# Performance work log

Measured on AMD Instinct MI355X. Metric: run time of the kernel, lower is better.

Reference implementation:

```python
import jax, jax.numpy as jnp
import numpy as np

B, C3, Dz, H, W = 2, 128, 32, 24, 24
C2, K = 96, 8
E, NH = 256, 4
HD = E // NH
BETA_ADJ = 0.5
EPS = 1e-5
TOPO_HIDDEN = 64


def setup_inputs() -> dict:
    key = jax.random.key(0)
    ks = jax.random.split(key, 10)
    def n(k, shape, s=0.02):
        return jax.random.normal(k, shape, jnp.float32) * s
    return {
        "F3": jax.random.normal(ks[0], (B, C3, Dz, H, W), jnp.float32),
        "F2": jax.random.normal(ks[1], (B, C2, H, W, K), jnp.float32),
        "Wq": n(ks[2], (C3, E)),
        "Wk": n(ks[3], (C2, E)),
        "Wv": n(ks[4], (C2, E)),
        "Wp": n(ks[5], (E, C3)),
        "ln_q_g": jnp.ones((E,), jnp.float32),
        "ln_q_b": jnp.zeros((E,), jnp.float32),
        "ln_kv_g": jnp.ones((E,), jnp.float32),
        "ln_kv_b": jnp.zeros((E,), jnp.float32),
        "conv1_w": n(ks[6], (TOPO_HIDDEN, C2, 3, 3)),
        "bn_g": jnp.ones((TOPO_HIDDEN,), jnp.float32),
        "bn_b": jnp.zeros((TOPO_HIDDEN,), jnp.float32),
        "conv2_w": n(ks[7], (1, TOPO_HIDDEN, 1, 1)),
        "conv2_b": jnp.zeros((1,), jnp.float32),
        "lam": jnp.asarray(0.3, jnp.float32),
        "D0": 128,
        "slab": 16,
    }


def _layernorm(x, g, b):
    m = jnp.mean(x, -1, keepdims=True)
    v = jnp.mean(jnp.square(x - m), -1, keepdims=True)
    return (x - m) * jax.lax.rsqrt(v + EPS) * g + b


def _conv2d(x, w, pad):
    return jax.lax.conv_general_dilated(
        x, w, (1, 1), [(pad, pad), (pad, pad)],
        dimension_numbers=("NCHW", "OIHW", "NCHW"))


def _forward(F3, F2, Wq, Wk, Wv, Wp, ln_q_g, ln_q_b, ln_kv_g, ln_kv_b,
             conv1_w, bn_g, bn_b, conv2_w, conv2_b, lam, D0, slab):
    HW = H * W
    # static slab-index map (D0, slab are Python ints)
    z0 = np.round(np.linspace(0.0, D0 - 1, Dz)).astype(np.int64)
    k_index = np.clip(z0 // slab, 0, K - 1)

    # ---- TopoPriorHead2D (BatchNorm in eval mode, default running stats 0/1) ----
    f2_bkchw = jnp.transpose(F2, (0, 4, 1, 2, 3)).reshape(B * K, C2, H, W)
    h = _conv2d(f2_bkchw, conv1_w, 1)
    h = h * (bn_g / np.float32(np.sqrt(1.0 + EPS)))[None, :, None, None] + bn_b[None, :, None, None]
    h = jax.nn.relu(h)
    p_pred = _conv2d(h, conv2_w, 0) + conv2_b[None, :, None, None]  # [B*K,1,H,W]
    nei = jnp.ones((1, 1, 3, 3), jnp.float32).at[0, 0, 1, 1].set(0.0)
    ps_pred = _conv2d(p_pred, nei, 1)
    topo_map = (p_pred + 0.5 * ps_pred).reshape(B, K, HW)

    # ---- Q/K/V projections + LayerNorm ----
    x2 = jnp.transpose(F2, (0, 4, 2, 3, 1)).reshape(B, K, HW, C2)
    Kall = _layernorm(x2 @ Wk, ln_kv_g, ln_kv_b).reshape(B, K, HW, NH, HD)
    Vall = _layernorm(x2 @ Wv, ln_kv_g, ln_kv_b).reshape(B, K, HW, NH, HD)
    x3 = jnp.transpose(F3, (0, 2, 3, 4, 1)).reshape(B, Dz, HW, C3)
    Qall = _layernorm(x3 @ Wq, ln_q_g, ln_q_b).reshape(B, Dz, HW, NH, HD)

    Oh = jnp.zeros_like(Qall)
    scale = np.float32(1.0 / np.sqrt(HD))
    hw = np.arange(HW)
    for kk in range(K):
        z_ids = np.nonzero(k_index == kk)[0]
        if z_ids.size == 0:
            continue
        cand = [c for c in (kk - 1, kk, kk + 1) if 0 <= c < K]
        L = len(cand)
        slab_bias = jnp.asarray(np.concatenate(
            [np.full(HW, 0.0 if c == kk else -BETA_ADJ, np.float32) for c in cand]))
        Qg = Qall[:, z_ids]                                    # [B,Ds,HW,NH,HD]
        Kc = Kall[:, np.asarray(cand)].reshape(B, L * HW, NH, HD)
        Vc = Vall[:, np.asarray(cand)].reshape(B, L * HW, NH, HD)
        # [B,NH,Ds,HW,M]
        logits = jnp.einsum('bdphc,bmhc->bhdpm', Qg, Kc) * scale
        logits = logits + slab_bias
        # diagonal topo boost: query pixel p attends to same pixel p in slab cand[j]
        diag = jnp.zeros((B, HW, L * HW), logits.dtype)
        for j, c in enumerate(cand):
            diag = diag.at[:, hw, j * HW + hw].add(lam * topo_map[:, c])
        logits = logits + diag[:, None, None]
        attn = jax.nn.softmax(logits, axis=-1)
        Og = jnp.einsum('bhdpm,bmhc->bdphc', attn, Vc)         # [B,Ds,HW,NH,HD]
        Oh = Oh.at[:, z_ids].set(Og)

    Oall = Oh.reshape(B, Dz, HW, E) @ Wp                        # [B,D,HW,C3]
    Oall = jnp.transpose(Oall.reshape(B, Dz, H, W, C3), (0, 4, 1, 2, 3))
    return F3 + Oall


def reference(F3, F2, Wq, Wk, Wv, Wp, ln_q_g, ln_q_b, ln_kv_g, ln_kv_b,
              conv1_w, bn_g, bn_b, conv2_w, conv2_b, lam, D0, slab):
    return _forward(F3, F2, Wq, Wk, Wv, Wp, ln_q_g, ln_q_b, ln_kv_g, ln_kv_b,
                    conv1_w, bn_g, bn_b, conv2_w, conv2_b, lam, D0, slab)
```

## Files before the change

### kernel.cpp

```cpp
#include <hip/hip_runtime.h>

typedef float f32x4 __attribute__((ext_vector_type(4)));
typedef __bf16 bf16x8 __attribute__((ext_vector_type(8)));
typedef unsigned short ushort_t;

#define DEV_INLINE __device__ __forceinline__

constexpr int B_N  = 2;
constexpr int C3_N = 128;
constexpr int C2_N = 96;
constexpr int DZ_N = 32;
constexpr int H_N  = 24;
constexpr int W_N  = 24;
constexpr int K_N  = 8;
constexpr int E_N  = 256;
constexpr int HW_N = 576;

DEV_INLINE unsigned short f2bf(float x) {
  union { __bf16 b; unsigned short u; } v;
  v.b = (__bf16)x;
  return v.u;
}

__global__ __launch_bounds__(384) void topo_conv1(
    const float* __restrict__ F2, const float* __restrict__ W1,
    float* __restrict__ Hp) {
  const int bid = blockIdx.x;
  const int cc = bid & 3;
  const int tg = (bid >> 2) & 3;
  const int bk = bid >> 4;
  const int b = bk >> 3, k = bk & 7;
  const int tid = threadIdx.x;
  const int y = tid >> 4;
  const int tq = tid & 15;

  __shared__ float simg[8][26][28];
  __shared__ float sw[16 * 97];

  float acc[24];
#pragma unroll
  for (int i = 0; i < 24; i++) acc[i] = 0.f;

  float* simgf = &simg[0][0][0];
  for (int i = tid; i < 8 * 26 * 28; i += 384) simgf[i] = 0.f;
  __syncthreads();

  for (int ch = 0; ch < 3; ch++) {
    if (ch) __syncthreads();
    const int c0 = cc * 24 + ch * 8;
    for (int i = tid; i < 8 * 24 * 24; i += 384) {
      int c = i / 576, p = i - c * 576;
      int yy = p / 24, xx = p - yy * 24;
      simg[c][yy + 1][xx + 1] =
          F2[(((b * C2_N + c0 + c) * H_N + yy) * W_N + xx) * K_N + k];
    }
    for (int i = tid; i < 16 * 72; i += 384) {
      int t2 = i / 72, rest = i - t2 * 72;
      int c = rest / 9, q = rest - c * 9;
      sw[t2 * 97 + c * 12 + q] =
          W1[(tg * 16 + t2) * (C2_N * 9) + (c0 + c) * 9 + q];
    }
    __syncthreads();
#pragma unroll 1
    for (int c = 0; c < 8; c++) {
      float w[9];
#pragma unroll
      for (int q = 0; q < 9; q++) w[q] = sw[tq * 97 + c * 12 + q];
#pragma unroll
      for (int dy = 0; dy < 3; dy++) {
        float r[28];
#pragma unroll
        for (int g = 0; g < 7; g++)
          *(float4*)&r[g * 4] = *(const float4*)&simg[c][y + dy][g * 4];
#pragma unroll
        for (int dx = 0; dx < 3; dx++) {
          float wv = w[dy * 3 + dx];
#pragma unroll
          for (int xx = 0; xx < 24; xx++)
            acc[xx] = fmaf(wv, r[xx + dx], acc[xx]);
        }
      }
    }
  }
  const int t = tg * 16 + tq;
  float* dst = &Hp[((cc * 16 + bk) * 64 + t) * HW_N + y * 24];
#pragma unroll
  for (int xx = 0; xx < 24; xx++) dst[xx] = acc[xx];
}

__global__ __launch_bounds__(576) void topo_mid(
    const float* __restrict__ Hp, const float* __restrict__ bn_g,
    const float* __restrict__ bn_b, const float* __restrict__ W2,
    float* __restrict__ part) {
  const int bid = blockIdx.x;
  const int tg = bid & 3, bk = bid >> 2;
  const int p = threadIdx.x;
  const float inv = rsqrtf(1.0f + 1e-5f);
  float acc = 0.f;
#pragma unroll 1
  for (int tt = 0; tt < 16; tt++) {
    const int t = tg * 16 + tt;
    float v = 0.f;
#pragma unroll
    for (int c4 = 0; c4 < 4; c4++)
      v += Hp[((c4 * 16 + bk) * 64 + t) * HW_N + p];
    acc = fmaf(W2[t], fmaxf(fmaf(bn_g[t] * inv, v, bn_b[t]), 0.f), acc);
  }
  part[(bk * 4 + tg) * HW_N + p] = acc;
}

__global__ __launch_bounds__(576) void topo_final2(
    const float* __restrict__ part, const float* __restrict__ b2,
    float* __restrict__ topo) {
  const int bk = blockIdx.x;
  const int p = threadIdx.x;
  __shared__ float pp[26][28];
  float* ppf = &pp[0][0];
  for (int i = p; i < 26 * 28; i += 576) ppf[i] = 0.f;
  float acc = b2[0];
#pragma unroll
  for (int tg = 0; tg < 4; tg++) acc += part[(bk * 4 + tg) * HW_N + p];
  __syncthreads();
  pp[p / 24 + 1][p % 24 + 1] = acc;
  __syncthreads();
  const int yy = p / 24 + 1, xx = p % 24 + 1;
  float s = pp[yy-1][xx-1] + pp[yy-1][xx] + pp[yy-1][xx+1]
          + pp[yy][xx-1]                  + pp[yy][xx+1]
          + pp[yy+1][xx-1] + pp[yy+1][xx] + pp[yy+1][xx+1];
  topo[bk * HW_N + p] = acc + 0.5f * s;
}

__global__ __launch_bounds__(256) void pack_all(
    const float* __restrict__ Wq, const float* __restrict__ Wk,
    const float* __restrict__ Wv, const float* __restrict__ Wp,
    ushort_t* __restrict__ Wqp, ushort_t* __restrict__ Wkp,
    ushort_t* __restrict__ Wvp, ushort_t* __restrict__ Wpp) {
  const int bblk = blockIdx.x, t = threadIdx.x;
  if (bblk < 256) {
    if (t < 128) Wqp[bblk * 128 + t] = f2bf(Wq[t * 256 + bblk]);
  } else if (bblk < 512) {
    const int n = bblk - 256;
    if (t < 96) Wkp[n * 96 + t] = f2bf(Wk[t * 256 + n]);
  } else if (bblk < 768) {
    const int n = bblk - 512;
    if (t < 96) Wvp[n * 96 + t] = f2bf(Wv[t * 256 + n]);
  } else {
    const int c = bblk - 768;
    Wpp[c * 256 + t] = f2bf(Wp[t * 128 + c]);
  }
}

template <int CIN, int MODE>
__global__ __launch_bounds__(256) void proj_mfma(
    const float* __restrict__ src, const ushort_t* __restrict__ Wpk,
    void* __restrict__ outp, const float* __restrict__ g,
    const float* __restrict__ bb,
    int outer, int bStride, int oStride, int pStride, int cStride) {
  __shared__ ushort_t sA[64 * 128];
  __shared__ int sRB[64];
  const int tid = threadIdx.x;
  const int rowG = blockIdx.x * 64;
  if (tid < 64) {
    int rr = rowG + tid;
    int b2 = rr / (outer * HW_N);
    int rem = rr - b2 * outer * HW_N;
    int o = rem / HW_N;
    int p = rem - o * HW_N;
    sRB[tid] = b2 * bStride + o * oStride + p * pStride;
  }
  __syncthreads();
  {
    const int r = tid & 63, kg = tid >> 6;
    constexpr int KC = CIN / 4;
    const float* s0 = src + sRB[r];
#pragma unroll
    for (int i = 0; i < KC; i += 2) {
      const int k = kg * KC + i;
      const float x0 = s0[k * cStride];
      const float x1 = s0[(k + 1) * cStride];
      const unsigned pr = (unsigned)f2bf(x0) | ((unsigned)f2bf(x1) << 16);
      ((unsigned*)sA)[r * 64 + (((k >> 3) + r) & 15) * 4 + ((k & 7) >> 1)] = pr;
    }
  }
  __syncthreads();
  const int wv = tid >> 6, lane = tid & 63;
  const int quad = lane >> 4, col = lane & 15;
  const int m = wv * 16 + col;
  constexpr int KS = CIN / 32;
  bf16x8 xb[KS];
#pragma unroll
  for (int ks = 0; ks < KS; ks++)
    xb[ks] = *(const bf16x8*)&sA[m * 128 + (((ks * 4 + quad) + m) & 15) * 8];
  f32x4 acc[16];
#pragma unroll
  for (int nt = 0; nt < 16; nt++) {
    const ushort_t* wrow = Wpk + (nt * 16 + col) * CIN + quad * 8;
    f32x4 a = (f32x4){0.f, 0.f, 0.f, 0.f};
#pragma unroll
    for (int ks = 0; ks < KS; ks++) {
      bf16x8 wf = *(const bf16x8*)&wrow[ks * 32];
      a = __builtin_amdgcn_mfma_f32_16x16x32_bf16(wf, xb[ks], a, 0, 0, 0);
    }
    acc[nt] = a;
  }
  const int mrow = rowG + m;
  if (MODE == 0) {
    float* dst = (float*)outp + (size_t)mrow * E_N;
#pragma unroll
    for (int nt = 0; nt < 16; nt++)
      *(f32x4*)&dst[nt * 16 + quad * 4] = acc[nt];
  } else {
    float s = 0.f;
#pragma unroll
    for (int nt = 0; nt < 16; nt++)
      s += acc[nt][0] + acc[nt][1] + acc[nt][2] + acc[nt][3];
    s += __shfl_xor(s, 16); s += __shfl_xor(s, 32);
    const float mean = s * (1.f / 256.f);
    float v = 0.f;
#pragma unroll
    for (int nt = 0; nt < 16; nt++)
#pragma unroll
      for (int r = 0; r < 4; r++) {
        const float d = acc[nt][r] - mean;
        v += d * d;
      }
    v += __shfl_xor(v, 16); v += __shfl_xor(v, 32);
    const float rstd = rsqrtf(v * (1.f / 256.f) + 1e-5f);
    if (MODE == 1) {
      const float QS = 0.18033688f;
      ushort_t* dst = (ushort_t*)outp + (size_t)mrow * E_N;
#pragma unroll
      for (int nt = 0; nt < 16; nt++) {
        const int n0 = nt * 16 + quad * 4;
        const float4 gv = *(const float4*)&g[n0];
        const float4 bv = *(const float4*)&bb[n0];
        ushort4 o;
        o.x = f2bf(QS * fmaf((acc[nt][0] - mean) * rstd, gv.x, bv.x));
        o.y = f2bf(QS * fmaf((acc[nt][1] - mean) * rstd, gv.y, bv.y));
        o.z = f2bf(QS * fmaf((acc[nt][2] - mean) * rstd, gv.z, bv.z));
        o.w = f2bf(QS * fmaf((acc[nt][3] - mean) * rstd, gv.w, bv.w));
        *(ushort4*)&dst[n0] = o;
      }
    }
  }
}

__global__ __launch_bounds__(256) void proj_kv(
    const float* __restrict__ F2, const ushort_t* __restrict__ Wkp,
    const ushort_t* __restrict__ Wvp, ushort_t* __restrict__ Kpk,
    ushort_t* __restrict__ Vtp, const float* __restrict__ g,
    const float* __restrict__ bb) {
  __shared__ ushort_t sA[64 * 128];
  __shared__ ushort_t sT[64][264];
  const int tid = threadIdx.x;
  const int rowG = blockIdx.x * 64;
  {
    const int r = tid & 63, kg = tid >> 6;
    const int rr = rowG + r;
    const int b2 = rr / (K_N * HW_N);
    const int rem = rr - b2 * (K_N * HW_N);
    const int k = rem / HW_N;
    const int p = rem - k * HW_N;
    const float* s0 = F2 + (size_t)b2 * (C2_N * HW_N * K_N) + k + p * K_N;
#pragma unroll
    for (int i = 0; i < 24; i += 2) {
      const int kk = kg * 24 + i;
      const float x0 = s0[kk * (HW_N * K_N)];
      const float x1 = s0[(kk + 1) * (HW_N * K_N)];
      const unsigned pr = (unsigned)f2bf(x0) | ((unsigned)f2bf(x1) << 16);
      ((unsigned*)sA)[r * 64 + (((kk >> 3) + r) & 15) * 4 + ((kk & 7) >> 1)] = pr;
    }
  }
  __syncthreads();
  const int wv = tid >> 6, lane = tid & 63;
  const int quad = lane >> 4, col = lane & 15;
  const int m = wv * 16 + col;
  bf16x8 xb[3];
#pragma unroll
  for (int ks = 0; ks < 3; ks++)
    xb[ks] = *(const bf16x8*)&sA[m * 128 + (((ks * 4 + quad) + m) & 15) * 8];

  const int mrow = rowG + m;
  const int bk = mrow / HW_N;
  const int p = mrow - bk * HW_N;
  const int pc = p >> 6, mm = p & 63;

  {
    f32x4 acc[16];
#pragma unroll
    for (int nt = 0; nt < 16; nt++) {
      const ushort_t* wrow = Wkp + (nt * 16 + col) * 96 + quad * 8;
      f32x4 a = (f32x4){0.f, 0.f, 0.f, 0.f};
#pragma unroll
      for (int ks = 0; ks < 3; ks++) {
        bf16x8 wf = *(const bf16x8*)&wrow[ks * 32];
        a = __builtin_amdgcn_mfma_f32_16x16x32_bf16(wf, xb[ks], a, 0, 0, 0);
      }
      acc[nt] = a;
    }
    float s = 0.f;
#pragma unroll
    for (int nt = 0; nt < 16; nt++)
      s += acc[nt][0] + acc[nt][1] + acc[nt][2] + acc[nt][3];
    s += __shfl_xor(s, 16); s += __shfl_xor(s, 32);
    const float mean = s * (1.f / 256.f);
    float v = 0.f;
#pragma unroll
    for (int nt = 0; nt < 16; nt++)
#pragma unroll
      for (int r = 0; r < 4; r++) {
        const float d = acc[nt][r] - mean;
        v += d * d;
      }
    v += __shfl_xor(v, 16); v += __shfl_xor(v, 32);
    const float rstd = rsqrtf(v * (1.f / 256.f) + 1e-5f);
#pragma unroll
    for (int nt = 0; nt < 16; nt++) {
      const int n0 = nt * 16 + quad * 4;
      const float4 gv = *(const float4*)&g[n0];
      const float4 bv = *(const float4*)&bb[n0];
      ushort4 o;
      o.x = f2bf(fmaf((acc[nt][0] - mean) * rstd, gv.x, bv.x));
      o.y = f2bf(fmaf((acc[nt][1] - mean) * rstd, gv.y, bv.y));
      o.z = f2bf(fmaf((acc[nt][2] - mean) * rstd, gv.z, bv.z));
      o.w = f2bf(fmaf((acc[nt][3] - mean) * rstd, gv.w, bv.w));
      const int h = nt >> 2;
      const int grp = ((nt & 3) * 2 + (quad >> 1)) ^ (mm & 7);
      ushort_t* dst = Kpk +
          ((size_t)((bk * 4 + h) * 9 + pc)) * 4096 +
          mm * 64 + grp * 8 + (quad & 1) * 4;
      *(ushort4*)dst = o;
    }
  }

  {
    f32x4 acc[16];
#pragma unroll
    for (int nt = 0; nt < 16; nt++) {
      const ushort_t* wrow = Wvp + (nt * 16 + col) * 96 + quad * 8;
      f32x4 a = (f32x4){0.f, 0.f, 0.f, 0.f};
#pragma unroll
      for (int ks = 0; ks < 3; ks++) {
        bf16x8 wf = *(const bf16x8*)&wrow[ks * 32];
        a = __builtin_amdgcn_mfma_f32_16x16x32_bf16(wf, xb[ks], a, 0, 0, 0);
      }
      acc[nt] = a;
    }
    float s = 0.f;
#pragma unroll
    for (int nt = 0; nt < 16; nt++)
      s += acc[nt][0] + acc[nt][1] + acc[nt][2] + acc[nt][3];
    s += __shfl_xor(s, 16); s += __shfl_xor(s, 32);
    const float mean = s * (1.f / 256.f);
    float v = 0.f;
#pragma unroll
    for (int nt = 0; nt < 16; nt++)
#pragma unroll
      for (int r = 0; r < 4; r++) {
        const float d = acc[nt][r] - mean;
        v += d * d;
      }
    v += __shfl_xor(v, 16); v += __shfl_xor(v, 32);
    const float rstd = rsqrtf(v * (1.f / 256.f) + 1e-5f);
#pragma unroll
    for (int nt = 0; nt < 16; nt++) {
      const int n0 = nt * 16 + quad * 4;
      const float4 gv = *(const float4*)&g[n0];
      const float4 bv = *(const float4*)&bb[n0];
      ushort4 o;
      o.x = f2bf(fmaf((acc[nt][0] - mean) * rstd, gv.x, bv.x));
      o.y = f2bf(fmaf((acc[nt][1] - mean) * rstd, gv.y, bv.y));
      o.z = f2bf(fmaf((acc[nt][2] - mean) * rstd, gv.z, bv.z));
      o.w = f2bf(fmaf((acc[nt][3] - mean) * rstd, gv.w, bv.w));
      *(ushort4*)&sT[m][n0] = o;
    }
  }
  __syncthreads();
  const int hh = tid >> 6, d = tid & 63;
  __attribute__((aligned(16))) ushort_t tmp[64];
#pragma unroll
  for (int k = 0; k < 64; k++) {
    const int pk = (k & 32) + ((k & 4) << 2) + ((k & 24) >> 1) + (k & 3);
    tmp[k] = sT[pk][hh * 64 + d];
  }
  const int chunk = (bk * 4 + hh) * 9 + pc;
  uint4* dst = (uint4*)&Vtp[chunk * 4096 + d * 64];
  const int sw = d & 7;
#pragma unroll
  for (int gg = 0; gg < 8; gg++) dst[gg ^ sw] = ((const uint4*)tmp)[gg];
}

__global__ __launch_bounds__(256) void attn_kernel(
    const ushort_t* __restrict__ Qbf, const ushort_t* __restrict__ Kpk,
    const ushort_t* __restrict__ Vtp, const float* __restrict__ topo,
    const float* __restrict__ lamp, const int* __restrict__ D0p,
    const int* __restrict__ slabp, ushort_t* __restrict__ Obf) {
  const int bid = blockIdx.x;
  const int hb = bid & 7;
  const int h = hb & 3, b = hb >> 2;
  const int zp = (bid >> 3) & 15;
  const int pb = bid >> 7;
  const int p0 = pb * 64;
  const int tid = threadIdx.x;
  const int w = tid >> 6, lane = tid & 63;
  const int quad = lane >> 4, col = lane & 15;
  const int z = zp * 2 + (w >> 1);
  const int th = w & 1;

  const float LOG2E = 1.44269504f;
  const float lam2 = lamp[0] * LOG2E;
  const int D0 = D0p[0], slab = slabp[0];
  const float step = (float)(D0 - 1) / (float)(DZ_N - 1);

  int kkw, kka, kkb;
  {
    int z0 = (int)floorf(fmaf((float)z, step, 0.5f));
    int kv = z0 / slab;
    kkw = kv < 0 ? 0 : (kv > K_N - 1 ? K_N - 1 : kv);
    int z0a = (int)floorf(fmaf((float)(zp * 2), step, 0.5f));
    int z0b = (int)floorf(fmaf((float)(zp * 2 + 1), step, 0.5f));
    int ka = z0a / slab; ka = ka < 0 ? 0 : (ka > K_N - 1 ? K_N - 1 : ka);
    int kb = z0b / slab; kb = kb < 0 ? 0 : (kb > K_N - 1 ? K_N - 1 : kb);
    kka = ka < kb ? ka : kb;
    kkb = ka < kb ? kb : ka;
  }
  const int c_lo = (kka - 1) < 0 ? 0 : (kka - 1);
  const int c_hi = (kkb + 1) > (K_N - 1) ? (K_N - 1) : (kkb + 1);

  __shared__ ushort_t sKV[2][8192];

  auto issue_fill = [&](int buf, int c, int pc) {
    const size_t cb = ((size_t)(((b * K_N + c) * 4 + h) * 9) + pc) * 4096;
#pragma unroll
    for (int j = 0; j < 4; j++) {
      const int seg = (w << 2) + j;
      const ushort_t* gsrc = (w < 2)
          ? (Kpk + cb + seg * 512 + lane * 8)
          : (Vtp + cb + (seg - 8) * 512 + lane * 8);
      ushort_t* ldst = &sKV[buf][seg * 512];
      __builtin_amdgcn_global_load_lds(
          (const __attribute__((address_space(1))) void*)gsrc,
          (__attribute__((address_space(3))) void*)ldst, 16, 0, 0);
    }
  };

  union { ushort_t u[8]; bf16x8 v; } uo;
#pragma unroll
  for (int i = 0; i < 8; i++) uo.u[i] = 0x3F80;
  const bf16x8 vone = uo.v;

  bf16x8 bq[2][2];
  const int qrow0 = (b * DZ_N + z) * HW_N + p0 + th * 32;
#pragma unroll
  for (int t = 0; t < 2; t++) {
    const ushort_t* qp = &Qbf[(qrow0 + t * 16 + col) * E_N + h * 64 + quad * 8];
    bq[t][0] = *(const bf16x8*)qp;
    bq[t][1] = *(const bf16x8*)(qp + 32);
  }

  f32x4 oacc[2][4];
#pragma unroll
  for (int t = 0; t < 2; t++)
#pragma unroll
    for (int dt = 0; dt < 4; dt++) oacc[t][dt] = (f32x4){0.f, 0.f, 0.f, 0.f};
  f32x4 lacc[2];
  lacc[0] = (f32x4){0.f, 0.f, 0.f, 0.f};
  lacc[1] = (f32x4){0.f, 0.f, 0.f, 0.f};

  const int s7 = col & 7;
  const int o1 = (quad ^ s7) * 8;
  const int o2 = ((quad + 4) ^ s7) * 8;

  int buf = 0;
  issue_fill(0, c_lo, 0);

  for (int c = c_lo; c <= c_hi; c++) {
    const bool act = (c >= kkw - 1) && (c <= kkw + 1);
    const float biasE2 = ((c == kkw) ? -20.0f : -20.5f) * LOG2E;
    const f32x4 bias4 = (f32x4){biasE2, biasE2, biasE2, biasE2};
    const float* topoc = &topo[(b * K_N + c) * HW_N + p0];
#pragma unroll 1
    for (int pc = 0; pc < 9; pc++) {
      __syncthreads();
      {
        int pc2 = pc + 1, c2 = c;
        if (pc2 == 9) { pc2 = 0; c2 = c + 1; }
        if (c2 <= c_hi) issue_fill(buf ^ 1, c2, pc2);
      }
      const ushort_t* sKb = &sKV[buf][0];
      const ushort_t* sVb = &sKV[buf][4096];
      buf ^= 1;
      if (!act) continue;

      bf16x8 ka[4][2];
#pragma unroll
      for (int kt = 0; kt < 4; kt++) {
        const ushort_t* kr = sKb + (kt * 16 + col) * 64;
        ka[kt][0] = *(const bf16x8*)(kr + o1);
        ka[kt][1] = *(const bf16x8*)(kr + o2);
      }

      bf16x8 pfrag[2][2];
#pragma unroll
      for (int t = 0; t < 2; t++) {
        f32x4 sv[4];
#pragma unroll
        for (int kt = 0; kt < 4; kt++) {
          f32x4 acc = __builtin_amdgcn_mfma_f32_16x16x32_bf16(
              ka[kt][0], bq[t][0], bias4, 0, 0, 0);
          acc = __builtin_amdgcn_mfma_f32_16x16x32_bf16(
              ka[kt][1], bq[t][1], acc, 0, 0, 0);
          sv[kt] = acc;
        }
        float xv[4][4];
#pragma unroll
        for (int kt = 0; kt < 4; kt++)
#pragma unroll
          for (int r = 0; r < 4; r++)
            xv[kt][r] = sv[kt][r];
        if (pc == pb) {
          const int ctt = th * 2 + t;
          const float tv2 = lam2 * topoc[th * 32 + t * 16 + col];
          const bool qok = ((col >> 2) == quad);
#pragma unroll
          for (int kt = 0; kt < 4; kt++)
#pragma unroll
            for (int r = 0; r < 4; r++)
              xv[kt][r] += (qok && kt == ctt && (col & 3) == r) ? tv2 : 0.f;
        }
        float ev[4][4];
#pragma unroll
        for (int kt = 0; kt < 4; kt++)
#pragma unroll
          for (int r = 0; r < 4; r++)
            ev[kt][r] = __builtin_amdgcn_exp2f(xv[kt][r]);
#pragma unroll
        for (int f = 0; f < 2; f++) {
          union { uint4 u; bf16x8 v; } pk;
          pk.u.x = __builtin_amdgcn_perm(__float_as_uint(ev[f*2][1]),
                                         __float_as_uint(ev[f*2][0]), 0x07060302u);
          pk.u.y = __builtin_amdgcn_perm(__float_as_uint(ev[f*2][3]),
                                         __float_as_uint(ev[f*2][2]), 0x07060302u);
          pk.u.z = __builtin_amdgcn_perm(__float_as_uint(ev[f*2+1][1]),
                                         __float_as_uint(ev[f*2+1][0]), 0x07060302u);
          pk.u.w = __builtin_amdgcn_perm(__float_as_uint(ev[f*2+1][3]),
                                         __float_as_uint(ev[f*2+1][2]), 0x07060302u);
          pfrag[t][f] = pk.v;
        }
        lacc[t] = __builtin_amdgcn_mfma_f32_16x16x32_bf16(
            vone, pfrag[t][0], lacc[t], 0, 0, 0);
        lacc[t] = __builtin_amdgcn_mfma_f32_16x16x32_bf16(
            vone, pfrag[t][1], lacc[t], 0, 0, 0);
      }

#pragma unroll
      for (int dt = 0; dt < 4; dt++) {
        const ushort_t* vr = sVb + (dt * 16 + col) * 64;
        bf16x8 va0 = *(const bf16x8*)(vr + o1);
        bf16x8 va1 = *(const bf16x8*)(vr + o2);
#pragma unroll
        for (int t = 0; t < 2; t++) {
          oacc[t][dt] = __builtin_amdgcn_mfma_f32_16x16x32_bf16(va0, pfrag[t][0], oacc[t][dt], 0, 0, 0);
          oacc[t][dt] = __builtin_amdgcn_mfma_f32_16x16x32_bf16(va1, pfrag[t][1], oacc[t][dt], 0, 0, 0);
        }
      }
    }
  }

#pragma unroll
  for (int t = 0; t < 2; t++) {
    const float invl = 1.f / lacc[t][0];
    const int row = qrow0 + t * 16 + col;
    ushort_t* orow = &Obf[(size_t)row * E_N + h * 64];
#pragma unroll
    for (int dt = 0; dt < 4; dt++) {
      ushort4 o;
      o.x = f2bf(oacc[t][dt][0] * invl);
      o.y = f2bf(oacc[t][dt][1] * invl);
      o.z = f2bf(oacc[t][dt][2] * invl);
      o.w = f2bf(oacc[t][dt][3] * invl);
      *(ushort4*)&orow[dt * 16 + quad * 4] = o;
    }
  }
}

__global__ __launch_bounds__(256) void out_proj_mfma(
    const ushort_t* __restrict__ Obf, const ushort_t* __restrict__ Wpp,
    const float* __restrict__ F3, float* __restrict__ outp) {
  __shared__ float sOut[64][129];
  const int tid = threadIdx.x;
  const int rowG = blockIdx.x * 64;
  const int wv = tid >> 6, lane = tid & 63;
  const int quad = lane >> 4, col = lane & 15;

  const ushort_t* xrow = &Obf[(size_t)(rowG + wv * 16 + col) * E_N + quad * 8];
  bf16x8 af[8];
#pragma unroll
  for (int ks = 0; ks < 8; ks++) af[ks] = *(const bf16x8*)&xrow[ks * 32];

#pragma unroll
  for (int nt = 0; nt < 8; nt++) {
    const ushort_t* wrow = &Wpp[(nt * 16 + col) * 256 + quad * 8];
    f32x4 a = (f32x4){0.f, 0.f, 0.f, 0.f};
#pragma unroll
    for (int ks = 0; ks < 8; ks++) {
      bf16x8 wf = *(const bf16x8*)&wrow[ks * 32];
      a = __builtin_amdgcn_mfma_f32_16x16x32_bf16(af[ks], wf, a, 0, 0, 0);
    }
#pragma unroll
    for (int r = 0; r < 4; r++)
      sOut[wv * 16 + quad * 4 + r][nt * 16 + col] = a[r];
  }
  __syncthreads();
  const int b = rowG / (DZ_N * HW_N);
  const int rem = rowG - b * DZ_N * HW_N;
  const int z = rem / HW_N;
  const int pp0 = rem - z * HW_N;
  const int pl = tid & 63, cg = tid >> 6;
  for (int c = cg * 32; c < cg * 32 + 32; c++) {
    const int gidx = ((b * C3_N + c) * DZ_N + z) * HW_N + pp0 + pl;
    outp[gidx] = F3[gidx] + sOut[pl][c];
  }
}

extern "C" void kernel_launch(void* const* d_in, const int* in_sizes, int n_in,
                              void* d_out, int out_size, void* d_ws, size_t ws_size,
                              hipStream_t stream) {
  (void)in_sizes; (void)n_in; (void)out_size; (void)ws_size;
  const float* F3      = (const float*)d_in[0];
  const float* F2      = (const float*)d_in[1];
  const float* Wq      = (const float*)d_in[2];
  const float* Wk      = (const float*)d_in[3];
  const float* Wv      = (const float*)d_in[4];
  const float* Wp      = (const float*)d_in[5];
  const float* ln_q_g  = (const float*)d_in[6];
  const float* ln_q_b  = (const float*)d_in[7];
  const float* ln_kv_g = (const float*)d_in[8];
  const float* ln_kv_b = (const float*)d_in[9];
  const float* conv1_w = (const float*)d_in[10];
  const float* bn_g    = (const float*)d_in[11];
  const float* bn_b    = (const float*)d_in[12];
  const float* conv2_w = (const float*)d_in[13];
  const float* conv2_b = (const float*)d_in[14];
  const float* lam     = (const float*)d_in[15];
  const int*   D0      = (const int*)d_in[16];
  const int*   slab    = (const int*)d_in[17];
  float* out = (float*)d_out;

  char* ws = (char*)d_ws;
  size_t off = 0;
  auto alloc = [&](size_t bytes) {
    void* p = ws + off;
    off += (bytes + 255) & ~(size_t)255;
    return p;
  };
  const int QROWS = B_N * DZ_N * HW_N;
  const int KVROWS = B_N * K_N * HW_N;
  ushort_t* Qbf = (ushort_t*)alloc((size_t)QROWS * E_N * 2);
  ushort_t* Kpk = (ushort_t*)alloc((size_t)KVROWS * E_N * 2);
  ushort_t* Vtp = (ushort_t*)alloc((size_t)KVROWS * E_N * 2);
  ushort_t* Obf = (ushort_t*)alloc((size_t)QROWS * E_N * 2);
  float* topo = (float*)alloc((size_t)B_N * K_N * HW_N * 4);
  float* part = (float*)alloc((size_t)64 * HW_N * 4);
  ushort_t* Wqp = (ushort_t*)alloc(256 * 128 * 2);
  ushort_t* Wkp = (ushort_t*)alloc(256 * 96 * 2);
  ushort_t* Wvp = (ushort_t*)alloc(256 * 96 * 2);
  ushort_t* Wpp = (ushort_t*)alloc(128 * 256 * 2);
  float* Hp = (float*)Obf;

  pack_all<<<896, 256, 0, stream>>>(Wq, Wk, Wv, Wp, Wqp, Wkp, Wvp, Wpp);
  topo_conv1<<<256, 384, 0, stream>>>(F2, conv1_w, Hp);
  topo_mid<<<64, 576, 0, stream>>>(Hp, bn_g, bn_b, conv2_w, part);
  topo_final2<<<16, 576, 0, stream>>>(part, conv2_b, topo);
  proj_mfma<128, 1><<<QROWS / 64, 256, 0, stream>>>(
      F3, Wqp, Qbf, ln_q_g, ln_q_b,
      DZ_N, C3_N * DZ_N * HW_N, HW_N, 1, DZ_N * HW_N);
  proj_kv<<<KVROWS / 64, 256, 0, stream>>>(
      F2, Wkp, Wvp, Kpk, Vtp, ln_kv_g, ln_kv_b);
  attn_kernel<<<1152, 256, 0, stream>>>(
      Qbf, Kpk, Vtp, topo, lam, D0, slab, Obf);
  out_proj_mfma<<<QROWS / 64, 256, 0, stream>>>(Obf, Wpp, F3, out);
}
```

Before: 301.0 us.

## Merge weight packing into conv1, fuse topo tail, combine Q and KV projections

Weight packing now runs as extra blocks inside the conv1 kernel, and the two topo reduction kernels become a single kernel with 16 blocks. The Q and KV projection kernels are merged into one launch that branches on block index. Together this cuts the launch count from eight to five and lets independent work share a grid. The cost is that the topo tail has far less parallelism (16 blocks each looping over 64 channels), and the packing blocks carry the conv kernel's 384-thread size and shared-memory footprint.

```diff
diff --git a/kernel.cpp b/kernel.cpp
--- a/kernel.cpp
+++ b/kernel.cpp
@@ -22,10 +22,35 @@
   return v.u;
 }
 
-__global__ __launch_bounds__(384) void topo_conv1(
+__global__ __launch_bounds__(384) void pre_conv_pack(
     const float* __restrict__ F2, const float* __restrict__ W1,
-    float* __restrict__ Hp) {
-  const int bid = blockIdx.x;
+    float* __restrict__ Hp,
+    const float* __restrict__ Wq, const float* __restrict__ Wk,
+    const float* __restrict__ Wv, const float* __restrict__ Wp,
+    ushort_t* __restrict__ Wqp, ushort_t* __restrict__ Wkp,
+    ushort_t* __restrict__ Wvp, ushort_t* __restrict__ Wpp) {
+  __shared__ float simg[8][26][28];
+  __shared__ float sw[16 * 97];
+  const int bid0 = blockIdx.x;
+  if (bid0 >= 256) {
+    const int bblk = bid0 - 256, t = threadIdx.x;
+    if (t < 256) {
+      if (bblk < 256) {
+        if (t < 128) Wqp[bblk * 128 + t] = f2bf(Wq[t * 256 + bblk]);
+      } else if (bblk < 512) {
+        const int n = bblk - 256;
+        if (t < 96) Wkp[n * 96 + t] = f2bf(Wk[t * 256 + n]);
+      } else if (bblk < 768) {
+        const int n = bblk - 512;
+        if (t < 96) Wvp[n * 96 + t] = f2bf(Wv[t * 256 + n]);
+      } else {
+        const int c = bblk - 768;
+        Wpp[c * 256 + t] = f2bf(Wp[t * 128 + c]);
+      }
+    }
+    return;
+  }
+  const int bid = bid0;
   const int cc = bid & 3;
   const int tg = (bid >> 2) & 3;
   const int bk = bid >> 4;
@@ -33,9 +58,6 @@
   const int tid = threadIdx.x;
   const int y = tid >> 4;
   const int tq = tid & 15;
-
-  __shared__ float simg[8][26][28];
-  __shared__ float sw[16 * 97];
 
   float acc[24];
 #pragma unroll
@@ -88,38 +110,25 @@
   for (int xx = 0; xx < 24; xx++) dst[xx] = acc[xx];
 }
 
-__global__ __launch_bounds__(576) void topo_mid(
+__global__ __launch_bounds__(576) void topo_tail(
     const float* __restrict__ Hp, const float* __restrict__ bn_g,
     const float* __restrict__ bn_b, const float* __restrict__ W2,
-    float* __restrict__ part) {
-  const int bid = blockIdx.x;
-  const int tg = bid & 3, bk = bid >> 2;
-  const int p = threadIdx.x;
-  const float inv = rsqrtf(1.0f + 1e-5f);
-  float acc = 0.f;
-#pragma unroll 1
-  for (int tt = 0; tt < 16; tt++) {
-    const int t = tg * 16 + tt;
-    float v = 0.f;
-#pragma unroll
-    for (int c4 = 0; c4 < 4; c4++)
-      v += Hp[((c4 * 16 + bk) * 64 + t) * HW_N + p];
-    acc = fmaf(W2[t], fmaxf(fmaf(bn_g[t] * inv, v, bn_b[t]), 0.f), acc);
-  }
-  part[(bk * 4 + tg) * HW_N + p] = acc;
-}
-
-__global__ __launch_bounds__(576) void topo_final2(
-    const float* __restrict__ part, const float* __restrict__ b2,
-    float* __restrict__ topo) {
+    const float* __restrict__ b2, float* __restrict__ topo) {
   const int bk = blockIdx.x;
   const int p = threadIdx.x;
   __shared__ float pp[26][28];
   float* ppf = &pp[0][0];
   for (int i = p; i < 26 * 28; i += 576) ppf[i] = 0.f;
+  const float inv = rsqrtf(1.0f + 1e-5f);
   float acc = b2[0];
-#pragma unroll
-  for (int tg = 0; tg < 4; tg++) acc += part[(bk * 4 + tg) * HW_N + p];
+#pragma unroll 1
+  for (int t = 0; t < 64; t++) {
+    float v = 0.f;
+#pragma unroll
+    for (int c4 = 0; c4 < 4; c4++)
+      v += Hp[((c4 * 16 + bk) * 64 + t) * HW_N + p];
+    acc = fmaf(W2[t], fmaxf(fmaf(bn_g[t] * inv, v, bn_b[t]), 0.f), acc);
+  }
   __syncthreads();
   pp[p / 24 + 1][p % 24 + 1] = acc;
   __syncthreads();
@@ -130,86 +139,194 @@
   topo[bk * HW_N + p] = acc + 0.5f * s;
 }
 
-__global__ __launch_bounds__(256) void pack_all(
-    const float* __restrict__ Wq, const float* __restrict__ Wk,
-    const float* __restrict__ Wv, const float* __restrict__ Wp,
-    ushort_t* __restrict__ Wqp, ushort_t* __restrict__ Wkp,
-    ushort_t* __restrict__ Wvp, ushort_t* __restrict__ Wpp) {
-  const int bblk = blockIdx.x, t = threadIdx.x;
-  if (bblk < 256) {
-    if (t < 128) Wqp[bblk * 128 + t] = f2bf(Wq[t * 256 + bblk]);
-  } else if (bblk < 512) {
-    const int n = bblk - 256;
-    if (t < 96) Wkp[n * 96 + t] = f2bf(Wk[t * 256 + n]);
-  } else if (bblk < 768) {
-    const int n = bblk - 512;
-    if (t < 96) Wvp[n * 96 + t] = f2bf(Wv[t * 256 + n]);
+__global__ __launch_bounds__(256) void proj_all(
+    const float* __restrict__ F3, const float* __restrict__ F2,
+    const ushort_t* __restrict__ Wqp, const ushort_t* __restrict__ Wkp,
+    const ushort_t* __restrict__ Wvp,
+    ushort_t* __restrict__ Qbf, ushort_t* __restrict__ Kpk,
+    ushort_t* __restrict__ Vtp,
+    const float* __restrict__ ln_q_g, const float* __restrict__ ln_q_b,
+    const float* __restrict__ ln_kv_g, const float* __restrict__ ln_kv_b) {
+  __shared__ ushort_t sA[64 * 128];
+  __shared__ ushort_t sT[64][264];
+  const int tid = threadIdx.x;
+
+  if (blockIdx.x < 144) {
+    const int rowG = blockIdx.x * 64;
+    {
+      const int r = tid & 63, kg = tid >> 6;
+      const int rr = rowG + r;
+      const int b2 = rr / (K_N * HW_N);
+      const int rem = rr - b2 * (K_N * HW_N);
+      const int k = rem / HW_N;
+      const int p = rem - k * HW_N;
+      const float* s0 = F2 + (size_t)b2 * (C2_N * HW_N * K_N) + k + p * K_N;
+#pragma unroll
+      for (int i = 0; i < 24; i += 2) {
+        const int kk = kg * 24 + i;
+        const float x0 = s0[kk * (HW_N * K_N)];
+        const float x1 = s0[(kk + 1) * (HW_N * K_N)];
+        const unsigned pr = (unsigned)f2bf(x0) | ((unsigned)f2bf(x1) << 16);
+        ((unsigned*)sA)[r * 64 + (((kk >> 3) + r) & 15) * 4 + ((kk & 7) >> 1)] = pr;
+      }
+    }
+    __syncthreads();
+    const int wv = tid >> 6, lane = tid & 63;
+    const int quad = lane >> 4, col = lane & 15;
+    const int m = wv * 16 + col;
+    bf16x8 xb[3];
+#pragma unroll
+    for (int ks = 0; ks < 3; ks++)
+      xb[ks] = *(const bf16x8*)&sA[m * 128 + (((ks * 4 + quad) + m) & 15) * 8];
+
+    const int mrow = rowG + m;
+    const int bk = mrow / HW_N;
+    const int p = mrow - bk * HW_N;
+    const int pc = p >> 6, mm = p & 63;
+
+    {
+      f32x4 acc[16];
+#pragma unroll
+      for (int nt = 0; nt < 16; nt++) {
+        const ushort_t* wrow = Wkp + (nt * 16 + col) * 96 + quad * 8;
+        f32x4 a = (f32x4){0.f, 0.f, 0.f, 0.f};
+#pragma unroll
+        for (int ks = 0; ks < 3; ks++) {
+          bf16x8 wf = *(const bf16x8*)&wrow[ks * 32];
+          a = __builtin_amdgcn_mfma_f32_16x16x32_bf16(wf, xb[ks], a, 0, 0, 0);
+        }
+        acc[nt] = a;
+      }
+      float s = 0.f;
+#pragma unroll
+      for (int nt = 0; nt < 16; nt++)
+        s += acc[nt][0] + acc[nt][1] + acc[nt][2] + acc[nt][3];
+      s += __shfl_xor(s, 16); s += __shfl_xor(s, 32);
+      const float mean = s * (1.f / 256.f);
+      float v = 0.f;
+#pragma unroll
+      for (int nt = 0; nt < 16; nt++)
+#pragma unroll
+        for (int r = 0; r < 4; r++) {
+          const float d = acc[nt][r] - mean;
+          v += d * d;
+        }
+      v += __shfl_xor(v, 16); v += __shfl_xor(v, 32);
+      const float rstd = rsqrtf(v * (1.f / 256.f) + 1e-5f);
+#pragma unroll
+      for (int nt = 0; nt < 16; nt++) {
+        const int n0 = nt * 16 + quad * 4;
+        const float4 gv = *(const float4*)&ln_kv_g[n0];
+        const float4 bv = *(const float4*)&ln_kv_b[n0];
+        ushort4 o;
+        o.x = f2bf(fmaf((acc[nt][0] - mean) * rstd, gv.x, bv.x));
+        o.y = f2bf(fmaf((acc[nt][1] - mean) * rstd, gv.y, bv.y));
+        o.z = f2bf(fmaf((acc[nt][2] - mean) * rstd, gv.z, bv.z));
+        o.w = f2bf(fmaf((acc[nt][3] - mean) * rstd, gv.w, bv.w));
+        const int h = nt >> 2;
+        const int grp = ((nt & 3) * 2 + (quad >> 1)) ^ (mm & 7);
+        ushort_t* dst = Kpk +
+            ((size_t)((bk * 4 + h) * 9 + pc)) * 4096 +
+            mm * 64 + grp * 8 + (quad & 1) * 4;
+        *(ushort4*)dst = o;
+      }
+    }
+
+    {
+      f32x4 acc[16];
+#pragma unroll
+      for (int nt = 0; nt < 16; nt++) {
+        const ushort_t* wrow = Wvp + (nt * 16 + col) * 96 + quad * 8;
+        f32x4 a = (f32x4){0.f, 0.f, 0.f, 0.f};
+#pragma unroll
+        for (int ks = 0; ks < 3; ks++) {
+          bf16x8 wf = *(const bf16x8*)&wrow[ks * 32];
+          a = __builtin_amdgcn_mfma_f32_16x16x32_bf16(wf, xb[ks], a, 0, 0, 0);
+        }
+        acc[nt] = a;
+      }
+      float s = 0.f;
+#pragma unroll
+      for (int nt = 0; nt < 16; nt++)
+        s += acc[nt][0] + acc[nt][1] + acc[nt][2] + acc[nt][3];
+      s += __shfl_xor(s, 16); s += __shfl_xor(s, 32);
+      const float mean = s * (1.f / 256.f);
+      float v = 0.f;
+#pragma unroll
+      for (int nt = 0; nt < 16; nt++)
+#pragma unroll
+        for (int r = 0; r < 4; r++) {
+          const float d = acc[nt][r] - mean;
+          v += d * d;
+        }
+      v += __shfl_xor(v, 16); v += __shfl_xor(v, 32);
+      const float rstd = rsqrtf(v * (1.f / 256.f) + 1e-5f);
+#pragma unroll
+      for (int nt = 0; nt < 16; nt++) {
+        const int n0 = nt * 16 + quad * 4;
+        const float4 gv = *(const float4*)&ln_kv_g[n0];
+        const float4 bv = *(const float4*)&ln_kv_b[n0];
+        ushort4 o;
+        o.x = f2bf(fmaf((acc[nt][0] - mean) * rstd, gv.x, bv.x));
+        o.y = f2bf(fmaf((acc[nt][1] - mean) * rstd, gv.y, bv.y));
+        o.z = f2bf(fmaf((acc[nt][2] - mean) * rstd, gv.z, bv.z));
+        o.w = f2bf(fmaf((acc[nt][3] - mean) * rstd, gv.w, bv.w));
+        *(ushort4*)&sT[m][n0] = o;
+      }
+    }
+    __syncthreads();
+    const int hh = tid >> 6, d = tid & 63;
+    __attribute__((aligned(16))) ushort_t tmp[64];
+#pragma unroll
+    for (int k = 0; k < 64; k++) {
+      const int pk = (k & 32) + ((k & 4) << 2) + ((k & 24) >> 1) + (k & 3);
+      tmp[k] = sT[pk][hh * 64 + d];
+    }
+    const int chunk = (bk * 4 + hh) * 9 + pc;
+    uint4* dst = (uint4*)&Vtp[chunk * 4096 + d * 64];
+    const int sw = d & 7;
+#pragma unroll
+    for (int gg = 0; gg < 8; gg++) dst[gg ^ sw] = ((const uint4*)tmp)[gg];
   } else {
-    const int c = bblk - 768;
-    Wpp[c * 256 + t] = f2bf(Wp[t * 128 + c]);
-  }
-}
-
-template <int CIN, int MODE>
-__global__ __launch_bounds__(256) void proj_mfma(
-    const float* __restrict__ src, const ushort_t* __restrict__ Wpk,
-    void* __restrict__ outp, const float* __restrict__ g,
-    const float* __restrict__ bb,
-    int outer, int bStride, int oStride, int pStride, int cStride) {
-  __shared__ ushort_t sA[64 * 128];
-  __shared__ int sRB[64];
-  const int tid = threadIdx.x;
-  const int rowG = blockIdx.x * 64;
-  if (tid < 64) {
-    int rr = rowG + tid;
-    int b2 = rr / (outer * HW_N);
-    int rem = rr - b2 * outer * HW_N;
-    int o = rem / HW_N;
-    int p = rem - o * HW_N;
-    sRB[tid] = b2 * bStride + o * oStride + p * pStride;
-  }
-  __syncthreads();
-  {
-    const int r = tid & 63, kg = tid >> 6;
-    constexpr int KC = CIN / 4;
-    const float* s0 = src + sRB[r];
-#pragma unroll
-    for (int i = 0; i < KC; i += 2) {
-      const int k = kg * KC + i;
-      const float x0 = s0[k * cStride];
-      const float x1 = s0[(k + 1) * cStride];
-      const unsigned pr = (unsigned)f2bf(x0) | ((unsigned)f2bf(x1) << 16);
-      ((unsigned*)sA)[r * 64 + (((k >> 3) + r) & 15) * 4 + ((k & 7) >> 1)] = pr;
-    }
-  }
-  __syncthreads();
-  const int wv = tid >> 6, lane = tid & 63;
-  const int quad = lane >> 4, col = lane & 15;
-  const int m = wv * 16 + col;
-  constexpr int KS = CIN / 32;
-  bf16x8 xb[KS];
-#pragma unroll
-  for (int ks = 0; ks < KS; ks++)
-    xb[ks] = *(const bf16x8*)&sA[m * 128 + (((ks * 4 + quad) + m) & 15) * 8];
-  f32x4 acc[16];
-#pragma unroll
-  for (int nt = 0; nt < 16; nt++) {
-    const ushort_t* wrow = Wpk + (nt * 16 + col) * CIN + quad * 8;
-    f32x4 a = (f32x4){0.f, 0.f, 0.f, 0.f};
-#pragma unroll
-    for (int ks = 0; ks < KS; ks++) {
-      bf16x8 wf = *(const bf16x8*)&wrow[ks * 32];
-      a = __builtin_amdgcn_mfma_f32_16x16x32_bf16(wf, xb[ks], a, 0, 0, 0);
-    }
-    acc[nt] = a;
-  }
-  const int mrow = rowG + m;
-  if (MODE == 0) {
-    float* dst = (float*)outp + (size_t)mrow * E_N;
-#pragma unroll
-    for (int nt = 0; nt < 16; nt++)
-      *(f32x4*)&dst[nt * 16 + quad * 4] = acc[nt];
-  } else {
+    const int rowG = (blockIdx.x - 144) * 64;
+    {
+      const int r = tid & 63, kg = tid >> 6;
+      const int rr = rowG + r;
+      const int b2 = rr / (DZ_N * HW_N);
+      const int rem = rr - b2 * (DZ_N * HW_N);
+      const int o = rem / HW_N;
+      const int p = rem - o * HW_N;
+      const float* s0 = F3 + (size_t)b2 * (C3_N * DZ_N * HW_N) + o * HW_N + p;
+#pragma unroll
+      for (int i = 0; i < 32; i += 2) {
+        const int k = kg * 32 + i;
+        const float x0 = s0[(size_t)k * (DZ_N * HW_N)];
+        const float x1 = s0[(size_t)(k + 1) * (DZ_N * HW_N)];
+        const unsigned pr = (unsigned)f2bf(x0) | ((unsigned)f2bf(x1) << 16);
+        ((unsigned*)sA)[r * 64 + (((k >> 3) + r) & 15) * 4 + ((k & 7) >> 1)] = pr;
+      }
+    }
+    __syncthreads();
+    const int wv = tid >> 6, lane = tid & 63;
+    const int quad = lane >> 4, col = lane & 15;
+    const int m = wv * 16 + col;
+    bf16x8 xb[4];
+#pragma unroll
+    for (int ks = 0; ks < 4; ks++)
+      xb[ks] = *(const bf16x8*)&sA[m * 128 + (((ks * 4 + quad) + m) & 15) * 8];
+    f32x4 acc[16];
+#pragma unroll
+    for (int nt = 0; nt < 16; nt++) {
+      const ushort_t* wrow = Wqp + (nt * 16 + col) * 128 + quad * 8;
+      f32x4 a = (f32x4){0.f, 0.f, 0.f, 0.f};
+#pragma unroll
+      for (int ks = 0; ks < 4; ks++) {
+        bf16x8 wf = *(const bf16x8*)&wrow[ks * 32];
+        a = __builtin_amdgcn_mfma_f32_16x16x32_bf16(wf, xb[ks], a, 0, 0, 0);
+      }
+      acc[nt] = a;
+    }
+    const int mrow = rowG + m;
     float s = 0.f;
 #pragma unroll
     for (int nt = 0; nt < 16; nt++)
@@ -226,168 +343,21 @@
       }
     v += __shfl_xor(v, 16); v += __shfl_xor(v, 32);
     const float rstd = rsqrtf(v * (1.f / 256.f) + 1e-5f);
-    if (MODE == 1) {
-      const float QS = 0.18033688f;
-      ushort_t* dst = (ushort_t*)outp + (size_t)mrow * E_N;
-#pragma unroll
-      for (int nt = 0; nt < 16; nt++) {
-        const int n0 = nt * 16 + quad * 4;
-        const float4 gv = *(const float4*)&g[n0];
-        const float4 bv = *(const float4*)&bb[n0];
-        ushort4 o;
-        o.x = f2bf(QS * fmaf((acc[nt][0] - mean) * rstd, gv.x, bv.x));
-        o.y = f2bf(QS * fmaf((acc[nt][1] - mean) * rstd, gv.y, bv.y));
-        o.z = f2bf(QS * fmaf((acc[nt][2] - mean) * rstd, gv.z, bv.z));
-        o.w = f2bf(QS * fmaf((acc[nt][3] - mean) * rstd, gv.w, bv.w));
-        *(ushort4*)&dst[n0] = o;
-      }
-    }
-  }
-}
-
-__global__ __launch_bounds__(256) void proj_kv(
-    const float* __restrict__ F2, const ushort_t* __restrict__ Wkp,
-    const ushort_t* __restrict__ Wvp, ushort_t* __restrict__ Kpk,
-    ushort_t* __restrict__ Vtp, const float* __restrict__ g,
-    const float* __restrict__ bb) {
-  __shared__ ushort_t sA[64 * 128];
-  __shared__ ushort_t sT[64][264];
-  const int tid = threadIdx.x;
-  const int rowG = blockIdx.x * 64;
-  {
-    const int r = tid & 63, kg = tid >> 6;
-    const int rr = rowG + r;
-    const int b2 = rr / (K_N * HW_N);
-    const int rem = rr - b2 * (K_N * HW_N);
-    const int k = rem / HW_N;
-    const int p = rem - k * HW_N;
-    const float* s0 = F2 + (size_t)b2 * (C2_N * HW_N * K_N) + k + p * K_N;
-#pragma unroll
-    for (int i = 0; i < 24; i += 2) {
-      const int kk = kg * 24 + i;
-      const float x0 = s0[kk * (HW_N * K_N)];
-      const float x1 = s0[(kk + 1) * (HW_N * K_N)];
-      const unsigned pr = (unsigned)f2bf(x0) | ((unsigned)f2bf(x1) << 16);
-      ((unsigned*)sA)[r * 64 + (((kk >> 3) + r) & 15) * 4 + ((kk & 7) >> 1)] = pr;
-    }
-  }
-  __syncthreads();
-  const int wv = tid >> 6, lane = tid & 63;
-  const int quad = lane >> 4, col = lane & 15;
-  const int m = wv * 16 + col;
-  bf16x8 xb[3];
-#pragma unroll
-  for (int ks = 0; ks < 3; ks++)
-    xb[ks] = *(const bf16x8*)&sA[m * 128 + (((ks * 4 + quad) + m) & 15) * 8];
-
-  const int mrow = rowG + m;
-  const int bk = mrow / HW_N;
-  const int p = mrow - bk * HW_N;
-  const int pc = p >> 6, mm = p & 63;
-
-  {
-    f32x4 acc[16];
-#pragma unroll
-    for (int nt = 0; nt < 16; nt++) {
-      const ushort_t* wrow = Wkp + (nt * 16 + col) * 96 + quad * 8;
-      f32x4 a = (f32x4){0.f, 0.f, 0.f, 0.f};
-#pragma unroll
-      for (int ks = 0; ks < 3; ks++) {
-        bf16x8 wf = *(const bf16x8*)&wrow[ks * 32];
-        a = __builtin_amdgcn_mfma_f32_16x16x32_bf16(wf, xb[ks], a, 0, 0, 0);
-      }
-      acc[nt] = a;
-    }
-    float s = 0.f;
-#pragma unroll
-    for (int nt = 0; nt < 16; nt++)
-      s += acc[nt][0] + acc[nt][1] + acc[nt][2] + acc[nt][3];
-    s += __shfl_xor(s, 16); s += __shfl_xor(s, 32);
-    const float mean = s * (1.f / 256.f);
-    float v = 0.f;
-#pragma unroll
-    for (int nt = 0; nt < 16; nt++)
-#pragma unroll
-      for (int r = 0; r < 4; r++) {
-        const float d = acc[nt][r] - mean;
-        v += d * d;
-      }
-    v += __shfl_xor(v, 16); v += __shfl_xor(v, 32);
-    const float rstd = rsqrtf(v * (1.f / 256.f) + 1e-5f);
+    const float QS = 0.18033688f;
+    ushort_t* dst = Qbf + (size_t)mrow * E_N;
 #pragma unroll
     for (int nt = 0; nt < 16; nt++) {
       const int n0 = nt * 16 + quad * 4;
-      const float4 gv = *(const float4*)&g[n0];
-      const float4 bv = *(const float4*)&bb[n0];
+      const float4 gv = *(const float4*)&ln_q_g[n0];
+      const float4 bv = *(const float4*)&ln_q_b[n0];
       ushort4 o;
-      o.x = f2bf(fmaf((acc[nt][0] - mean) * rstd, gv.x, bv.x));
-      o.y = f2bf(fmaf((acc[nt][1] - mean) * rstd, gv.y, bv.y));
-      o.z = f2bf(fmaf((acc[nt][2] - mean) * rstd, gv.z, bv.z));
-      o.w = f2bf(fmaf((acc[nt][3] - mean) * rstd, gv.w, bv.w));
-      const int h = nt >> 2;
-      const int grp = ((nt & 3) * 2 + (quad >> 1)) ^ (mm & 7);
-      ushort_t* dst = Kpk +
-          ((size_t)((bk * 4 + h) * 9 + pc)) * 4096 +
-          mm * 64 + grp * 8 + (quad & 1) * 4;
-      *(ushort4*)dst = o;
-    }
-  }
-
-  {
-    f32x4 acc[16];
-#pragma unroll
-    for (int nt = 0; nt < 16; nt++) {
-      const ushort_t* wrow = Wvp + (nt * 16 + col) * 96 + quad * 8;
-      f32x4 a = (f32x4){0.f, 0.f, 0.f, 0.f};
-#pragma unroll
-      for (int ks = 0; ks < 3; ks++) {
-        bf16x8 wf = *(const bf16x8*)&wrow[ks * 32];
-        a = __builtin_amdgcn_mfma_f32_16x16x32_bf16(wf, xb[ks], a, 0, 0, 0);
-      }
-      acc[nt] = a;
-    }
-    float s = 0.f;
-#pragma unroll
-    for (int nt = 0; nt < 16; nt++)
-      s += acc[nt][0] + acc[nt][1] + acc[nt][2] + acc[nt][3];
-    s += __shfl_xor(s, 16); s += __shfl_xor(s, 32);
-    const float mean = s * (1.f / 256.f);
-    float v = 0.f;
-#pragma unroll
-    for (int nt = 0; nt < 16; nt++)
-#pragma unroll
-      for (int r = 0; r < 4; r++) {
-        const float d = acc[nt][r] - mean;
-        v += d * d;
-      }
-    v += __shfl_xor(v, 16); v += __shfl_xor(v, 32);
-    const float rstd = rsqrtf(v * (1.f / 256.f) + 1e-5f);
-#pragma unroll
-    for (int nt = 0; nt < 16; nt++) {
-      const int n0 = nt * 16 + quad * 4;
-      const float4 gv = *(const float4*)&g[n0];
-      const float4 bv = *(const float4*)&bb[n0];
-      ushort4 o;
-      o.x = f2bf(fmaf((acc[nt][0] - mean) * rstd, gv.x, bv.x));
-      o.y = f2bf(fmaf((acc[nt][1] - mean) * rstd, gv.y, bv.y));
-      o.z = f2bf(fmaf((acc[nt][2] - mean) * rstd, gv.z, bv.z));
-      o.w = f2bf(fmaf((acc[nt][3] - mean) * rstd, gv.w, bv.w));
-      *(ushort4*)&sT[m][n0] = o;
-    }
-  }
-  __syncthreads();
-  const int hh = tid >> 6, d = tid & 63;
-  __attribute__((aligned(16))) ushort_t tmp[64];
-#pragma unroll
-  for (int k = 0; k < 64; k++) {
-    const int pk = (k & 32) + ((k & 4) << 2) + ((k & 24) >> 1) + (k & 3);
-    tmp[k] = sT[pk][hh * 64 + d];
-  }
-  const int chunk = (bk * 4 + hh) * 9 + pc;
-  uint4* dst = (uint4*)&Vtp[chunk * 4096 + d * 64];
-  const int sw = d & 7;
-#pragma unroll
-  for (int gg = 0; gg < 8; gg++) dst[gg ^ sw] = ((const uint4*)tmp)[gg];
+      o.x = f2bf(QS * fmaf((acc[nt][0] - mean) * rstd, gv.x, bv.x));
+      o.y = f2bf(QS * fmaf((acc[nt][1] - mean) * rstd, gv.y, bv.y));
+      o.z = f2bf(QS * fmaf((acc[nt][2] - mean) * rstd, gv.z, bv.z));
+      o.w = f2bf(QS * fmaf((acc[nt][3] - mean) * rstd, gv.w, bv.w));
+      *(ushort4*)&dst[n0] = o;
+    }
+  }
 }
 
 __global__ __launch_bounds__(256) void attn_kernel(
@@ -661,22 +631,18 @@
   ushort_t* Vtp = (ushort_t*)alloc((size_t)KVROWS * E_N * 2);
   ushort_t* Obf = (ushort_t*)alloc((size_t)QROWS * E_N * 2);
   float* topo = (float*)alloc((size_t)B_N * K_N * HW_N * 4);
-  float* part = (float*)alloc((size_t)64 * HW_N * 4);
   ushort_t* Wqp = (ushort_t*)alloc(256 * 128 * 2);
   ushort_t* Wkp = (ushort_t*)alloc(256 * 96 * 2);
   ushort_t* Wvp = (ushort_t*)alloc(256 * 96 * 2);
   ushort_t* Wpp = (ushort_t*)alloc(128 * 256 * 2);
   float* Hp = (float*)Obf;
 
-  pack_all<<<896, 256, 0, stream>>>(Wq, Wk, Wv, Wp, Wqp, Wkp, Wvp, Wpp);
-  topo_conv1<<<256, 384, 0, stream>>>(F2, conv1_w, Hp);
-  topo_mid<<<64, 576, 0, stream>>>(Hp, bn_g, bn_b, conv2_w, part);
-  topo_final2<<<16, 576, 0, stream>>>(part, conv2_b, topo);
-  proj_mfma<128, 1><<<QROWS / 64, 256, 0, stream>>>(
-      F3, Wqp, Qbf, ln_q_g, ln_q_b,
-      DZ_N, C3_N * DZ_N * HW_N, HW_N, 1, DZ_N * HW_N);
-  proj_kv<<<KVROWS / 64, 256, 0, stream>>>(
-      F2, Wkp, Wvp, Kpk, Vtp, ln_kv_g, ln_kv_b);
+  pre_conv_pack<<<1152, 384, 0, stream>>>(
+      F2, conv1_w, Hp, Wq, Wk, Wv, Wp, Wqp, Wkp, Wvp, Wpp);
+  topo_tail<<<16, 576, 0, stream>>>(Hp, bn_g, bn_b, conv2_w, conv2_b, topo);
+  proj_all<<<720, 256, 0, stream>>>(
+      F3, F2, Wqp, Wkp, Wvp, Qbf, Kpk, Vtp,
+      ln_q_g, ln_q_b, ln_kv_g, ln_kv_b);
   attn_kernel<<<1152, 256, 0, stream>>>(
       Qbf, Kpk, Vtp, topo, lam, D0, slab, Obf);
   out_proj_mfma<<<QROWS / 64, 256, 0, stream>>>(Obf, Wpp, F3, out);
```

New measurement: 301.0 us. Within noise of the previous version (-0.0%).
